# Optimization experiments

Measured on AMD Instinct MI355X. Metric: run time of the kernel, lower is better.

The kernel has to match this reference:

```python
import jax, jax.numpy as jnp
import numpy as np

N = 2048      # num nodes
F = 64        # in_channels
H = 16        # hidden_channels
O = 8         # out_channels


def setup_inputs() -> dict:
    key = jax.random.key(0)
    ks = jax.random.split(key, 16)
    s = 0.2  # small init scale
    inp = {
        "x": jax.random.normal(ks[0], (N, F), jnp.float32),
        "node_distances": jax.random.uniform(ks[1], (N, N), jnp.float32) * 5.0,
        "normalization": jax.random.uniform(ks[2], (N, N), jnp.float32) + 0.5,
        # per-feature f MLPs (1 -> H -> H -> O), stacked over features
        "fW1": jax.random.normal(ks[3], (F, H), jnp.float32) * s,
        "fb1": jnp.zeros((F, H), jnp.float32),
        "fW2": jax.random.normal(ks[4], (F, H, H), jnp.float32) * s,  # [F, out, in]
        "fb2": jnp.zeros((F, H), jnp.float32),
        "fW3": jax.random.normal(ks[5], (F, O, H), jnp.float32) * s,  # [F, out, in]
        "fb3": jnp.zeros((F, O), jnp.float32),
        # shared m MLP (1 -> H -> H -> 1), limited_m=True
        "mW1": jax.random.normal(ks[6], (H,), jnp.float32) * s,
        "mb1": jnp.zeros((H,), jnp.float32),
        "mW2": jax.random.normal(ks[7], (H, H), jnp.float32) * s,    # [out, in]
        "mb2": jnp.zeros((H,), jnp.float32),
        "mW3": jax.random.normal(ks[8], (H,), jnp.float32) * s,
        "mb3": jnp.zeros((), jnp.float32),
    }
    return inp


def reference(x, node_distances, normalization,
              fW1, fb1, fW2, fb2, fW3, fb3,
              mW1, mb1, mW2, mb2, mW3, mb3):
    # ---- per-feature f MLPs, vectorized over all nodes and features ----
    # x: [N, F] -> h: [N, F, H]
    h = jax.nn.relu(x[:, :, None] * fW1[None] + fb1[None])
    h = jax.nn.relu(jnp.einsum('nfh,fgh->nfg', h, fW2) + fb2[None])
    fx = jnp.einsum('nfh,foh->nfo', h, fW3) + fb3[None]        # [N, F, O]
    f_sums = fx.sum(axis=1)                                    # [N, O]

    # ---- m MLP applied elementwise to all pairwise distances ----
    d = node_distances                                         # [N, N]
    hm = jax.nn.relu(d[:, :, None] * mW1 + mb1)                # [N, N, H]
    hm = jax.nn.relu(jnp.einsum('ijh,gh->ijg', hm, mW2) + mb2)
    m_out = jnp.einsum('ijh,h->ij', hm, mW3) + mb3             # [N, N] (out dim 1)

    # normalize_m=True, m output dim == 1
    m_norm = m_out / normalization                             # [N, N]

    # pred[i] = sum_j m_norm[i, j] * f_sums[j]
    return m_norm @ f_sums                                     # [N, O]
```

## Files before the change

kernel.cpp:

```cpp
#include <hip/hip_runtime.h>

#define NN 2048
#define FF 64
#define HH 16
#define OO 8

#define BIGF  1e30f
#define BIGTH 1e29f
#define MAXBP 288
#define BPPAD 512
#define ABPAD 320
#define GCELL 1024

__device__ inline int cell_of(float d)
{
    int k = (int)floorf(fmaf(d, 32.f, 512.f));
    return min(max(k, 0), GCELL - 1);
}
__device__ inline int keycell(float v)
{
    return (v > BIGTH) ? GCELL : cell_of(v);
}

__device__ inline void l1_pattern(float c, const float* w1, const float* b1,
                                  float* a1, float* v1)
{
#pragma unroll
    for (int h = 0; h < HH; ++h) {
        const float arg = fmaf(w1[h], c, b1[h]);
        const bool act = arg > 0.f;
        a1[h] = act ? w1[h] : 0.f;
        v1[h] = act ? b1[h] : 0.f;
    }
}

__device__ inline void l2_arg(float c, int g,
                              const float* w1, const float* b1,
                              const float* w2, const float* b2,
                              float& A, float& B)
{
    float a1[HH], v1[HH];
    l1_pattern(c, w1, b1, a1, v1);
    float Aa = 0.f, Bb = b2[g];
#pragma unroll
    for (int h = 0; h < HH; ++h) {
        Aa = fmaf(w2[g * HH + h], a1[h], Aa);
        Bb = fmaf(w2[g * HH + h], v1[h], Bb);
    }
    A = Aa; B = Bb;
}

__device__ inline void pwl_coeffs(float c,
                                  const float* w1, const float* b1,
                                  const float* w2, const float* b2,
                                  const float* w3, float b3,
                                  float& alpha, float& beta)
{
    float a1[HH], v1[HH];
    l1_pattern(c, w1, b1, a1, v1);
    float al = 0.f, be = b3;
#pragma unroll
    for (int g = 0; g < HH; ++g) {
        float A = 0.f, B = b2[g];
#pragma unroll
        for (int h = 0; h < HH; ++h) {
            A = fmaf(w2[g * HH + h], a1[h], A);
            B = fmaf(w2[g * HH + h], v1[h], B);
        }
        const bool act = fmaf(A, c, B) > 0.f;
        al = fmaf(w3[g], act ? A : 0.f, al);
        be = fmaf(w3[g], act ? B : 0.f, be);
    }
    alpha = al; beta = be;
}

__device__ inline float seg_midpoint(float L, float R)
{
    float c;
    if (L <= -BIGTH && R >= BIGTH) c = 2.5f;
    else if (L <= -BIGTH)          c = R - 1.f;
    else if (R >= BIGTH)           c = L + 1.f;
    else                           c = 0.5f * (L + R);
    return fminf(fmaxf(c, -20.f), 20.f);
}

__global__ __launch_bounds__(512) void setup_kernel(
    const float* __restrict__ x,
    const float* __restrict__ fW1, const float* __restrict__ fb1,
    const float* __restrict__ fW2, const float* __restrict__ fb2,
    const float* __restrict__ fW3, const float* __restrict__ fb3,
    const float* __restrict__ mW1, const float* __restrict__ mb1,
    const float* __restrict__ mW2, const float* __restrict__ mb2,
    const float* __restrict__ mW3, const float* __restrict__ mb3,
    float* __restrict__ part,
    float* __restrict__ bp_out, float* __restrict__ ab_out,
    float* __restrict__ cell4_out, float* __restrict__ cellb_out)
{
    const int tid = threadIdx.x;

    if (blockIdx.x < 256) {
        __shared__ float sw1[HH], sb1[HH], sw2[HH * HH], sb2[HH], sw3[OO * HH], sb3[OO];
        const int f = blockIdx.x & 63;

        if (tid < HH) {
            sw1[tid] = fW1[f * HH + tid];
            sb1[tid] = fb1[f * HH + tid];
            sb2[tid] = fb2[f * HH + tid];
        }
        if (tid < HH * HH) sw2[tid] = fW2[f * HH * HH + tid];
        if (tid < OO * HH) sw3[tid] = fW3[f * OO * HH + tid];
        if (tid < OO)      sb3[tid] = fb3[f * OO + tid];
        __syncthreads();

        const int n = (blockIdx.x >> 6) * 512 + tid;
        const float xv = x[n * FF + f];

        float h1[HH];
#pragma unroll
        for (int h = 0; h < HH; ++h)
            h1[h] = fmaxf(fmaf(xv, sw1[h], sb1[h]), 0.f);

        float h2[HH];
#pragma unroll
        for (int g = 0; g < HH; ++g) {
            float a = sb2[g];
#pragma unroll
            for (int h = 0; h < HH; ++h) a = fmaf(sw2[g * HH + h], h1[h], a);
            h2[g] = fmaxf(a, 0.f);
        }

#pragma unroll
        for (int o = 0; o < OO; ++o) {
            float a = sb3[o];
#pragma unroll
            for (int h = 0; h < HH; ++h) a = fmaf(sw3[o * HH + h], h2[h], a);
            part[(n * FF + f) * OO + o] = a;
        }
        return;
    }

    __shared__ float w1[HH], b1[HH], w2[HH * HH], b2[HH], w3[HH];
    __shared__ float b3s;
    __shared__ float ends[18];
    __shared__ float cand[MAXBP];
    __shared__ float sorted[BPPAD];
    __shared__ float t16s[HH];
    __shared__ float sal[ABPAD], sbe[ABPAD];

    if (tid < HH) { w1[tid] = mW1[tid]; b1[tid] = mb1[tid]; b2[tid] = mb2[tid]; w3[tid] = mW3[tid]; }
    if (tid < HH * HH) w2[tid] = mW2[tid];
    if (tid == 0) b3s = mb3[0];
    sorted[tid] = BIGF;
    __syncthreads();

    if (tid < HH) {
        const float w = w1[tid];
        const float t = -b1[tid] / w;
        cand[tid] = (w != 0.f && t > -10.f && t < 10.f) ? t : BIGF;
    }
    __syncthreads();
    if (tid < HH) {
        const float my = cand[tid];
        int r = 0;
        for (int k = 0; k < HH; ++k) {
            const float o = cand[k];
            r += (o < my) || (o == my && k < tid);
        }
        t16s[r] = my;
    }
    __syncthreads();
    if (tid == 0)  ends[0] = -BIGF;
    if (tid < HH)  ends[tid + 1] = t16s[tid];
    if (tid == 0)  ends[17] = BIGF;
    __syncthreads();

    if (tid < 17 * HH) {
        const int iv = tid >> 4;
        const int g  = tid & 15;
        const float L = ends[iv], R = ends[iv + 1];
        float xx = BIGF;
        if (L < BIGTH) {
            const float c = seg_midpoint(L, R);
            float A, B;
            l2_arg(c, g, w1, b1, w2, b2, A, B);
            const float t = -B / A;
            if (t > L && t < R && t > -10.f && t < 10.f) xx = t;
        }
        cand[HH + tid] = xx;
    }
    __syncthreads();

    if (tid < MAXBP) {
        const float my = cand[tid];
        int r = 0;
        for (int k = 0; k < MAXBP; ++k) {
            const float o = cand[k];
            r += (o < my) || (o == my && k < tid);
        }
        sorted[r] = my;
    }
    __syncthreads();

    bp_out[tid] = sorted[tid];

    if (tid < ABPAD) {
        float al = 0.f, be = 0.f;
        if (tid <= MAXBP) {
            const float L = (tid == 0)    ? -BIGF : sorted[tid - 1];
            const float R = (tid < MAXBP) ? sorted[tid] : BIGF;
            const float c = seg_midpoint(L, R);
            pwl_coeffs(c, w1, b1, w2, b2, w3, b3s, al, be);
        }
        sal[tid] = al; sbe[tid] = be;
        ab_out[tid] = al;
        ab_out[ABPAD + tid] = be;
    }
    __syncthreads();

    for (int k = tid; k < GCELL; k += 512) {
        int base = 0, nxt = 0;
#pragma unroll
        for (int st = 256; st >= 1; st >>= 1) {
            base += (keycell(sorted[base + st - 1]) < k)     ? st : 0;
            nxt  += (keycell(sorted[nxt  + st - 1]) < k + 1) ? st : 0;
        }
        const int cnt = nxt - base;
        float4 r; float bk;
        if (cnt == 0) {
            r.x = sal[base]; r.y = sbe[base]; r.z = r.x; r.w = r.y;
            bk = -BIGF;
        } else {
            const float bmin = sorted[base];
            const float bmax = sorted[nxt - 1];
            if (bmin == bmax) {
                r.x = sal[base];       r.y = sbe[base];
                r.z = sal[base + cnt]; r.w = sbe[base + cnt];
                bk = bmin;
            } else {
                r.x = r.y = r.z = r.w = 0.f;
                bk = __int_as_float(0x7fc00000);
            }
        }
        reinterpret_cast<float4*>(cell4_out)[k] = r;
        cellb_out[k] = bk;
    }
}

__global__ __launch_bounds__(256) void fsum_reduce(
    const float* __restrict__ part, float* __restrict__ f_sums)
{
    const int n = blockIdx.x * 4 + (threadIdx.x >> 6);
    const int f = threadIdx.x & 63;
    const float4* p = reinterpret_cast<const float4*>(part + (n * FF + f) * OO);
    float4 a = p[0];
    float4 b = p[1];
#pragma unroll
    for (int off = 32; off > 0; off >>= 1) {
        a.x += __shfl_down(a.x, off, 64);
        a.y += __shfl_down(a.y, off, 64);
        a.z += __shfl_down(a.z, off, 64);
        a.w += __shfl_down(a.w, off, 64);
        b.x += __shfl_down(b.x, off, 64);
        b.y += __shfl_down(b.y, off, 64);
        b.z += __shfl_down(b.z, off, 64);
        b.w += __shfl_down(b.w, off, 64);
    }
    if (f == 0) {
        float4* q = reinterpret_cast<float4*>(f_sums + n * OO);
        q[0] = a;
        q[1] = b;
    }
}

__global__ __launch_bounds__(256) void mnet_kernel(
    const float* __restrict__ d, const float* __restrict__ norm,
    const float* __restrict__ f_sums,
    const float* __restrict__ bp_g, const float* __restrict__ ab_g,
    const float* __restrict__ cell4_g, const float* __restrict__ cellb_g,
    float* __restrict__ out)
{
    __shared__ float4 sc4[GCELL];
    __shared__ float  scb[GCELL];
    __shared__ float  sbp[BPPAD], sal[ABPAD], sbe[ABPAD];
    const int tid = threadIdx.x;

    for (int k = tid; k < GCELL; k += 256) {
        sc4[k] = reinterpret_cast<const float4*>(cell4_g)[k];
        scb[k] = cellb_g[k];
    }
    for (int k = tid; k < BPPAD; k += 256) sbp[k] = bp_g[k];
    for (int k = tid; k < ABPAD; k += 256) { sal[k] = ab_g[k]; sbe[k] = ab_g[ABPAD + k]; }
    __syncthreads();

    const int w = tid >> 6;
    const int lane = tid & 63;
    const int i = blockIdx.x * 4 + w;

    const float* drow = d + (size_t)i * NN;
    const float* nrow = norm + (size_t)i * NN;

    float acc[OO];
#pragma unroll
    for (int o = 0; o < OO; ++o) acc[o] = 0.f;

#pragma unroll
    for (int it = 0; it < NN / 256; ++it) {
        const int j0 = (it * 64 + lane) * 4;
        const float4 dv4 = *reinterpret_cast<const float4*>(drow + j0);
        const float4 nv4 = *reinterpret_cast<const float4*>(nrow + j0);
        const float dvs[4] = {dv4.x, dv4.y, dv4.z, dv4.w};
        const float nvs[4] = {nv4.x, nv4.y, nv4.z, nv4.w};
#pragma unroll
        for (int e = 0; e < 4; ++e) {
            const float dv = dvs[e];
            const int k = cell_of(dv);
            const float4 r = sc4[k];
            const float bk = scb[k];
            float al = (dv < bk) ? r.x : r.z;
            float be = (dv < bk) ? r.y : r.w;
            if (bk != bk) {
                int lo = 0;
#pragma unroll
                for (int st = 256; st >= 1; st >>= 1)
                    lo += (sbp[lo + st - 1] <= dv) ? st : 0;
                al = sal[lo]; be = sbe[lo];
            }
            const float mn = fmaf(al, dv, be) * __builtin_amdgcn_rcpf(nvs[e]);
            const float4 f0 = *reinterpret_cast<const float4*>(f_sums + (j0 + e) * OO);
            const float4 f1 = *reinterpret_cast<const float4*>(f_sums + (j0 + e) * OO + 4);
            acc[0] = fmaf(mn, f0.x, acc[0]);
            acc[1] = fmaf(mn, f0.y, acc[1]);
            acc[2] = fmaf(mn, f0.z, acc[2]);
            acc[3] = fmaf(mn, f0.w, acc[3]);
            acc[4] = fmaf(mn, f1.x, acc[4]);
            acc[5] = fmaf(mn, f1.y, acc[5]);
            acc[6] = fmaf(mn, f1.z, acc[6]);
            acc[7] = fmaf(mn, f1.w, acc[7]);
        }
    }

#pragma unroll
    for (int off = 32; off > 0; off >>= 1) {
#pragma unroll
        for (int o = 0; o < OO; ++o) acc[o] += __shfl_down(acc[o], off, 64);
    }
    if (lane == 0) {
#pragma unroll
        for (int o = 0; o < OO; ++o) out[i * OO + o] = acc[o];
    }
}

extern "C" void kernel_launch(void* const* d_in, const int* in_sizes, int n_in,
                              void* d_out, int out_size, void* d_ws, size_t ws_size,
                              hipStream_t stream)
{
    const float* x   = (const float*)d_in[0];
    const float* nd  = (const float*)d_in[1];
    const float* nm  = (const float*)d_in[2];
    const float* fW1 = (const float*)d_in[3];
    const float* fb1 = (const float*)d_in[4];
    const float* fW2 = (const float*)d_in[5];
    const float* fb2 = (const float*)d_in[6];
    const float* fW3 = (const float*)d_in[7];
    const float* fb3 = (const float*)d_in[8];
    const float* mW1 = (const float*)d_in[9];
    const float* mb1 = (const float*)d_in[10];
    const float* mW2 = (const float*)d_in[11];
    const float* mb2 = (const float*)d_in[12];
    const float* mW3 = (const float*)d_in[13];
    const float* mb3 = (const float*)d_in[14];
    float* out = (float*)d_out;

    float* part   = (float*)d_ws;
    float* f_sums = part + (size_t)NN * FF * OO;
    float* bp     = f_sums + (size_t)NN * OO;
    float* ab     = bp + BPPAD;
    float* cell4  = ab + 2 * ABPAD;
    float* cellb  = cell4 + 4 * GCELL;

    setup_kernel<<<257, 512, 0, stream>>>(
        x, fW1, fb1, fW2, fb2, fW3, fb3,
        mW1, mb1, mW2, mb2, mW3, mb3,
        part, bp, ab, cell4, cellb);
    fsum_reduce<<<512, 256, 0, stream>>>(part, f_sums);
    mnet_kernel<<<512, 256, 0, stream>>>(nd, nm, f_sums, bp, ab, cell4, cellb, out);
}
```

Before: 47.76 us.

## Assign one row per block and read lookup tables from global memory

The m-network kernel now gives each output row a whole 256-thread block instead of one wavefront, and launches NN blocks instead of 512. Each block combines its four wave partial sums through a small shared-memory reduction. The per-block staging of the ~20KB piecewise-linear lookup tables into LDS is removed; table lookups now go straight to global memory and rely on the cache. The f_sums loads are also issued up front to overlap their latency. This removes the table-staging cost and its barrier and adds parallelism, at the cost of scattered global/L1 gathers instead of LDS hits.

```diff
diff --git a/kernel.cpp b/kernel.cpp
--- a/kernel.cpp
+++ b/kernel.cpp
@@ -279,63 +279,55 @@
     const float* __restrict__ cell4_g, const float* __restrict__ cellb_g,
     float* __restrict__ out)
 {
-    __shared__ float4 sc4[GCELL];
-    __shared__ float  scb[GCELL];
-    __shared__ float  sbp[BPPAD], sal[ABPAD], sbe[ABPAD];
+    __shared__ float red[4][OO];
     const int tid = threadIdx.x;
-
-    for (int k = tid; k < GCELL; k += 256) {
-        sc4[k] = reinterpret_cast<const float4*>(cell4_g)[k];
-        scb[k] = cellb_g[k];
-    }
-    for (int k = tid; k < BPPAD; k += 256) sbp[k] = bp_g[k];
-    for (int k = tid; k < ABPAD; k += 256) { sal[k] = ab_g[k]; sbe[k] = ab_g[ABPAD + k]; }
-    __syncthreads();
-
-    const int w = tid >> 6;
-    const int lane = tid & 63;
-    const int i = blockIdx.x * 4 + w;
+    const int i = blockIdx.x;
 
     const float* drow = d + (size_t)i * NN;
     const float* nrow = norm + (size_t)i * NN;
+    const float4* c4 = reinterpret_cast<const float4*>(cell4_g);
 
     float acc[OO];
 #pragma unroll
     for (int o = 0; o < OO; ++o) acc[o] = 0.f;
 
 #pragma unroll
-    for (int it = 0; it < NN / 256; ++it) {
-        const int j0 = (it * 64 + lane) * 4;
+    for (int it = 0; it < 2; ++it) {
+        const int j0 = (it * 256 + tid) * 4;
         const float4 dv4 = *reinterpret_cast<const float4*>(drow + j0);
         const float4 nv4 = *reinterpret_cast<const float4*>(nrow + j0);
+        float4 fs[8];
+#pragma unroll
+        for (int e = 0; e < 4; ++e) {
+            fs[2 * e]     = *reinterpret_cast<const float4*>(f_sums + (j0 + e) * OO);
+            fs[2 * e + 1] = *reinterpret_cast<const float4*>(f_sums + (j0 + e) * OO + 4);
+        }
         const float dvs[4] = {dv4.x, dv4.y, dv4.z, dv4.w};
         const float nvs[4] = {nv4.x, nv4.y, nv4.z, nv4.w};
 #pragma unroll
         for (int e = 0; e < 4; ++e) {
             const float dv = dvs[e];
             const int k = cell_of(dv);
-            const float4 r = sc4[k];
-            const float bk = scb[k];
+            const float4 r = c4[k];
+            const float bk = cellb_g[k];
             float al = (dv < bk) ? r.x : r.z;
             float be = (dv < bk) ? r.y : r.w;
             if (bk != bk) {
                 int lo = 0;
 #pragma unroll
                 for (int st = 256; st >= 1; st >>= 1)
-                    lo += (sbp[lo + st - 1] <= dv) ? st : 0;
-                al = sal[lo]; be = sbe[lo];
+                    lo += (bp_g[lo + st - 1] <= dv) ? st : 0;
+                al = ab_g[lo]; be = ab_g[ABPAD + lo];
             }
             const float mn = fmaf(al, dv, be) * __builtin_amdgcn_rcpf(nvs[e]);
-            const float4 f0 = *reinterpret_cast<const float4*>(f_sums + (j0 + e) * OO);
-            const float4 f1 = *reinterpret_cast<const float4*>(f_sums + (j0 + e) * OO + 4);
-            acc[0] = fmaf(mn, f0.x, acc[0]);
-            acc[1] = fmaf(mn, f0.y, acc[1]);
-            acc[2] = fmaf(mn, f0.z, acc[2]);
-            acc[3] = fmaf(mn, f0.w, acc[3]);
-            acc[4] = fmaf(mn, f1.x, acc[4]);
-            acc[5] = fmaf(mn, f1.y, acc[5]);
-            acc[6] = fmaf(mn, f1.z, acc[6]);
-            acc[7] = fmaf(mn, f1.w, acc[7]);
+            acc[0] = fmaf(mn, fs[2 * e].x, acc[0]);
+            acc[1] = fmaf(mn, fs[2 * e].y, acc[1]);
+            acc[2] = fmaf(mn, fs[2 * e].z, acc[2]);
+            acc[3] = fmaf(mn, fs[2 * e].w, acc[3]);
+            acc[4] = fmaf(mn, fs[2 * e + 1].x, acc[4]);
+            acc[5] = fmaf(mn, fs[2 * e + 1].y, acc[5]);
+            acc[6] = fmaf(mn, fs[2 * e + 1].z, acc[6]);
+            acc[7] = fmaf(mn, fs[2 * e + 1].w, acc[7]);
         }
     }
 
@@ -344,9 +336,17 @@
 #pragma unroll
         for (int o = 0; o < OO; ++o) acc[o] += __shfl_down(acc[o], off, 64);
     }
+    const int wave = tid >> 6;
+    const int lane = tid & 63;
     if (lane == 0) {
 #pragma unroll
-        for (int o = 0; o < OO; ++o) out[i * OO + o] = acc[o];
+        for (int o = 0; o < OO; ++o) red[wave][o] = acc[o];
+    }
+    __syncthreads();
+    if (tid == 0) {
+#pragma unroll
+        for (int o = 0; o < OO; ++o)
+            out[i * OO + o] = red[0][o] + red[1][o] + red[2][o] + red[3][o];
     }
 }
 
@@ -383,5 +383,5 @@
         mW1, mb1, mW2, mb2, mW3, mb3,
         part, bp, ab, cell4, cellb);
     fsum_reduce<<<512, 256, 0, stream>>>(part, f_sums);
-    mnet_kernel<<<512, 256, 0, stream>>>(nd, nm, f_sums, bp, ab, cell4, cellb, out);
-}
+    mnet_kernel<<<NN, 256, 0, stream>>>(nd, nm, f_sums, bp, ab, cell4, cellb, out);
+}
```

Measured after the change: 49.70 us. 4.1% more time.
